# Optimization experiments

Hardware: AMD Instinct MI355X
Metric: run time of the kernel (lower is better)

The kernel has to match this reference:

```python
import jax, jax.numpy as jnp
import numpy as np

GRID_SIZE = 128
FEATURE_SIZE = 16
HIDDEN_SIZE = 64
N_POINTS = 2097152


def setup_inputs() -> dict:
    key = jax.random.key(0)
    ks = jax.random.split(key, 8)
    points = jax.random.uniform(ks[0], (N_POINTS, 3), dtype=jnp.float32)
    grid = jax.random.normal(ks[1], (GRID_SIZE, GRID_SIZE, GRID_SIZE, FEATURE_SIZE), dtype=jnp.float32)
    # torch nn.Linear default init: U(-1/sqrt(fan_in), 1/sqrt(fan_in))
    def linear(k, fan_in, fan_out):
        kw, kb = jax.random.split(k)
        bound = 1.0 / np.sqrt(fan_in)
        W = jax.random.uniform(kw, (fan_out, fan_in), minval=-bound, maxval=bound, dtype=jnp.float32)
        b = jax.random.uniform(kb, (fan_out,), minval=-bound, maxval=bound, dtype=jnp.float32)
        return W, b
    W1, b1 = linear(ks[2], FEATURE_SIZE, HIDDEN_SIZE)
    W2, b2 = linear(ks[3], HIDDEN_SIZE, HIDDEN_SIZE)
    W3, b3 = linear(ks[4], HIDDEN_SIZE, 1)
    return {"points": points, "grid": grid, "W1": W1, "b1": b1,
            "W2": W2, "b2": b2, "W3": W3, "b3": b3}


def reference(points, grid, W1, b1, W2, b2, W3, b3):
    gs = grid.shape[0]
    # nearest-grid-node index: scale to [0, gs-1], clamp, round
    p = jnp.clip(points * (gs - 1), 0.0, gs - 1)
    idx = jnp.round(p).astype(jnp.int32)  # (N, 3)
    feats = grid[idx[:, 0], idx[:, 1], idx[:, 2]]  # (N, F) gather
    h = jax.nn.relu(feats @ W1.T + b1)
    h = jax.nn.relu(h @ W2.T + b2)
    occ = jnp.tanh(h @ W3.T + b3)  # (N, 1)
    return occ
```

## Files before the change

kernel.cpp:

```cpp
#include <hip/hip_runtime.h>
#include <hip/hip_fp16.h>
#include <cstdint>
#include <cstddef>


typedef _Float16 half8 __attribute__((ext_vector_type(8)));
typedef float float4v __attribute__((ext_vector_type(4)));

__device__ inline uint32_t pack_f16x2(float a, float b) {
    union { _Float16 h[2]; uint32_t u; } v;
    v.h[0] = (_Float16)a;
    v.h[1] = (_Float16)b;
    return v.u;
}

__global__ __launch_bounds__(256) void occ_mlp_kernel(
    const float* __restrict__ pts,
    const float* __restrict__ grid,
    const float* __restrict__ W1, const float* __restrict__ b1,
    const float* __restrict__ W2, const float* __restrict__ b2,
    const float* __restrict__ W3, const float* __restrict__ b3,
    float* __restrict__ out, int nPoints)
{
    const int lane = threadIdx.x & 63;
    const int l15  = lane & 15;
    const int quad = lane >> 4;
    const int wavesPerBlock = blockDim.x >> 6;
    const int waveId = blockIdx.x * wavesPerBlock + (threadIdx.x >> 6);
    const int nWaves = gridDim.x * wavesPerBlock;

    half8 A1[4];
#pragma unroll
    for (int t = 0; t < 4; ++t) {
        half8 f = {};
        if (quad < 2) {
            const float* row = W1 + (16 * t + l15) * 16 + quad * 8;
#pragma unroll
            for (int j = 0; j < 8; ++j) f[j] = (_Float16)row[j];
        }
        A1[t] = f;
    }
    half8 A2[4][2];
#pragma unroll
    for (int t = 0; t < 4; ++t)
#pragma unroll
        for (int kk = 0; kk < 2; ++kk) {
            const float* row = W2 + (16 * t + l15) * 64 + 32 * kk + 8 * quad;
            half8 f;
#pragma unroll
            for (int j = 0; j < 8; ++j) f[j] = (_Float16)row[j];
            A2[t][kk] = f;
        }
    float4v bias1[4], bias2[4];
    float w3v[4][4];
#pragma unroll
    for (int t = 0; t < 4; ++t)
#pragma unroll
        for (int r = 0; r < 4; ++r) {
            int h = 16 * t + 4 * quad + r;
            bias1[t][r] = b1[h];
            bias2[t][r] = b2[h];
            w3v[t][r]   = W3[h];
        }
    const float bias3 = b3[0];

    const int src0 = l15 + 16 * ((2 * quad) & 3);
    const int src1 = l15 + 16 * ((2 * quad + 1) & 3);
    const bool sel = (quad >> 1) != 0;

    const int nTiles = (nPoints + 15) >> 4;
    for (int tile = waveId; tile < nTiles; tile += nWaves) {
        const int p = tile * 16 + l15;
        const int pc = p < nPoints ? p : nPoints - 1;

        const float px = pts[3 * pc + 0];
        const float py = pts[3 * pc + 1];
        const float pz = pts[3 * pc + 2];
        const int ix = (int)rintf(fminf(fmaxf(px * 127.0f, 0.0f), 127.0f));
        const int iy = (int)rintf(fminf(fmaxf(py * 127.0f, 0.0f), 127.0f));
        const int iz = (int)rintf(fminf(fmaxf(pz * 127.0f, 0.0f), 127.0f));
        const int ofs = ((((ix << 7) | iy) << 7) | iz) << 4;
        const float* g = grid + ofs;

        half8 bfrag = {};
        if (quad < 2) {
            const float4* gp = reinterpret_cast<const float4*>(g + quad * 8);
            const float4 f0 = gp[0];
            const float4 f1 = gp[1];
            bfrag[0] = (_Float16)f0.x; bfrag[1] = (_Float16)f0.y;
            bfrag[2] = (_Float16)f0.z; bfrag[3] = (_Float16)f0.w;
            bfrag[4] = (_Float16)f1.x; bfrag[5] = (_Float16)f1.y;
            bfrag[6] = (_Float16)f1.z; bfrag[7] = (_Float16)f1.w;
        }

        float4v C1[4];
#pragma unroll
        for (int t = 0; t < 4; ++t) {
            C1[t] = bias1[t];
            C1[t] = __builtin_amdgcn_mfma_f32_16x16x32_f16(A1[t], bfrag, C1[t], 0, 0, 0);
        }

        uint32_t P[4][2];
#pragma unroll
        for (int t = 0; t < 4; ++t) {
            const float v0 = fmaxf(C1[t][0], 0.0f);
            const float v1 = fmaxf(C1[t][1], 0.0f);
            const float v2 = fmaxf(C1[t][2], 0.0f);
            const float v3 = fmaxf(C1[t][3], 0.0f);
            P[t][0] = pack_f16x2(v0, v1);
            P[t][1] = pack_f16x2(v2, v3);
        }

        union Frag { uint32_t u[4]; half8 h; } B2[2];
#pragma unroll
        for (int kk = 0; kk < 2; ++kk) {
            const uint32_t x0a = (uint32_t)__shfl((int)P[2 * kk    ][0], src0);
            const uint32_t x0b = (uint32_t)__shfl((int)P[2 * kk + 1][0], src0);
            const uint32_t x1a = (uint32_t)__shfl((int)P[2 * kk    ][1], src0);
            const uint32_t x1b = (uint32_t)__shfl((int)P[2 * kk + 1][1], src0);
            const uint32_t y0a = (uint32_t)__shfl((int)P[2 * kk    ][0], src1);
            const uint32_t y0b = (uint32_t)__shfl((int)P[2 * kk + 1][0], src1);
            const uint32_t y1a = (uint32_t)__shfl((int)P[2 * kk    ][1], src1);
            const uint32_t y1b = (uint32_t)__shfl((int)P[2 * kk + 1][1], src1);
            B2[kk].u[0] = sel ? x0b : x0a;
            B2[kk].u[1] = sel ? x1b : x1a;
            B2[kk].u[2] = sel ? y0b : y0a;
            B2[kk].u[3] = sel ? y1b : y1a;
        }

        float4v C2[4];
#pragma unroll
        for (int t = 0; t < 4; ++t) C2[t] = bias2[t];
#pragma unroll
        for (int kk = 0; kk < 2; ++kk)
#pragma unroll
            for (int t = 0; t < 4; ++t)
                C2[t] = __builtin_amdgcn_mfma_f32_16x16x32_f16(A2[t][kk], B2[kk].h, C2[t], 0, 0, 0);

        float z = 0.0f;
#pragma unroll
        for (int t = 0; t < 4; ++t)
#pragma unroll
            for (int r = 0; r < 4; ++r)
                z = fmaf(fmaxf(C2[t][r], 0.0f), w3v[t][r], z);
        z += __shfl_xor(z, 16);
        z += __shfl_xor(z, 32);
        const float o = tanhf(z + bias3);
        if (lane < 16 && p < nPoints) out[p] = o;
    }
}

extern "C" void kernel_launch(void* const* d_in, const int* in_sizes, int n_in,
                              void* d_out, int out_size, void* d_ws, size_t ws_size,
                              hipStream_t stream)
{
    const float* pts  = (const float*)d_in[0];
    const float* grid = (const float*)d_in[1];
    const float* W1   = (const float*)d_in[2];
    const float* b1   = (const float*)d_in[3];
    const float* W2   = (const float*)d_in[4];
    const float* b2   = (const float*)d_in[5];
    const float* W3   = (const float*)d_in[6];
    const float* b3   = (const float*)d_in[7];
    float* out = (float*)d_out;
    const int nPoints = in_sizes[0] / 3;

    occ_mlp_kernel<<<dim3(2048), dim3(256), 0, stream>>>(
        pts, grid, W1, b1, W2, b2, W3, b3, out, nPoints);
}
```

Baseline: 286.7 us.

## Batch four point tiles per wave to overlap gathers and coalesce stores

Each wave now handles four 16-point tiles per iteration. It computes all four grid offsets and issues all eight random float4 gathers before any MFMA work, so more loads are in flight to hide gather latency. Outputs are collected so that all 64 lanes write one contiguous 64-float store, replacing four 16-lane stores. This raises register pressure from holding four tiles of gathered data, which may lower occupancy.

```diff
diff --git a/kernel.cpp b/kernel.cpp
--- a/kernel.cpp
+++ b/kernel.cpp
@@ -69,84 +69,102 @@
     const bool sel = (quad >> 1) != 0;
 
     const int nTiles = (nPoints + 15) >> 4;
-    for (int tile = waveId; tile < nTiles; tile += nWaves) {
-        const int p = tile * 16 + l15;
-        const int pc = p < nPoints ? p : nPoints - 1;
+    for (int tb = waveId * 4; tb < nTiles; tb += nWaves * 4) {
 
-        const float px = pts[3 * pc + 0];
-        const float py = pts[3 * pc + 1];
-        const float pz = pts[3 * pc + 2];
-        const int ix = (int)rintf(fminf(fmaxf(px * 127.0f, 0.0f), 127.0f));
-        const int iy = (int)rintf(fminf(fmaxf(py * 127.0f, 0.0f), 127.0f));
-        const int iz = (int)rintf(fminf(fmaxf(pz * 127.0f, 0.0f), 127.0f));
-        const int ofs = ((((ix << 7) | iy) << 7) | iz) << 4;
-        const float* g = grid + ofs;
-
-        half8 bfrag = {};
-        if (quad < 2) {
-            const float4* gp = reinterpret_cast<const float4*>(g + quad * 8);
-            const float4 f0 = gp[0];
-            const float4 f1 = gp[1];
-            bfrag[0] = (_Float16)f0.x; bfrag[1] = (_Float16)f0.y;
-            bfrag[2] = (_Float16)f0.z; bfrag[3] = (_Float16)f0.w;
-            bfrag[4] = (_Float16)f1.x; bfrag[5] = (_Float16)f1.y;
-            bfrag[6] = (_Float16)f1.z; bfrag[7] = (_Float16)f1.w;
+        int ofs[4];
+#pragma unroll
+        for (int u = 0; u < 4; ++u) {
+            int p = (tb + u) * 16 + l15;
+            int pc = p < nPoints ? p : nPoints - 1;
+            const float px = pts[3 * pc + 0];
+            const float py = pts[3 * pc + 1];
+            const float pz = pts[3 * pc + 2];
+            const int ix = (int)rintf(fminf(fmaxf(px * 127.0f, 0.0f), 127.0f));
+            const int iy = (int)rintf(fminf(fmaxf(py * 127.0f, 0.0f), 127.0f));
+            const int iz = (int)rintf(fminf(fmaxf(pz * 127.0f, 0.0f), 127.0f));
+            ofs[u] = ((((ix << 7) | iy) << 7) | iz) << 4;
         }
 
-        float4v C1[4];
+        float4 g0[4] = {}, g1[4] = {};
 #pragma unroll
-        for (int t = 0; t < 4; ++t) {
-            C1[t] = bias1[t];
-            C1[t] = __builtin_amdgcn_mfma_f32_16x16x32_f16(A1[t], bfrag, C1[t], 0, 0, 0);
+        for (int u = 0; u < 4; ++u) {
+            if (quad < 2) {
+                const float4* gp = reinterpret_cast<const float4*>(grid + ofs[u] + quad * 8);
+                g0[u] = gp[0];
+                g1[u] = gp[1];
+            }
         }
 
-        uint32_t P[4][2];
+        float o[4];
 #pragma unroll
-        for (int t = 0; t < 4; ++t) {
-            const float v0 = fmaxf(C1[t][0], 0.0f);
-            const float v1 = fmaxf(C1[t][1], 0.0f);
-            const float v2 = fmaxf(C1[t][2], 0.0f);
-            const float v3 = fmaxf(C1[t][3], 0.0f);
-            P[t][0] = pack_f16x2(v0, v1);
-            P[t][1] = pack_f16x2(v2, v3);
+        for (int u = 0; u < 4; ++u) {
+            half8 bfrag = {};
+            if (quad < 2) {
+                bfrag[0] = (_Float16)g0[u].x; bfrag[1] = (_Float16)g0[u].y;
+                bfrag[2] = (_Float16)g0[u].z; bfrag[3] = (_Float16)g0[u].w;
+                bfrag[4] = (_Float16)g1[u].x; bfrag[5] = (_Float16)g1[u].y;
+                bfrag[6] = (_Float16)g1[u].z; bfrag[7] = (_Float16)g1[u].w;
+            }
+
+            float4v C1[4];
+#pragma unroll
+            for (int t = 0; t < 4; ++t) {
+                C1[t] = bias1[t];
+                C1[t] = __builtin_amdgcn_mfma_f32_16x16x32_f16(A1[t], bfrag, C1[t], 0, 0, 0);
+            }
+
+            uint32_t P[4][2];
+#pragma unroll
+            for (int t = 0; t < 4; ++t) {
+                const float v0 = fmaxf(C1[t][0], 0.0f);
+                const float v1 = fmaxf(C1[t][1], 0.0f);
+                const float v2 = fmaxf(C1[t][2], 0.0f);
+                const float v3 = fmaxf(C1[t][3], 0.0f);
+                P[t][0] = pack_f16x2(v0, v1);
+                P[t][1] = pack_f16x2(v2, v3);
+            }
+
+            union Frag { uint32_t u[4]; half8 h; } B2[2];
+#pragma unroll
+            for (int kk = 0; kk < 2; ++kk) {
+                const uint32_t x0a = (uint32_t)__shfl((int)P[2 * kk    ][0], src0);
+                const uint32_t x0b = (uint32_t)__shfl((int)P[2 * kk + 1][0], src0);
+                const uint32_t x1a = (uint32_t)__shfl((int)P[2 * kk    ][1], src0);
+                const uint32_t x1b = (uint32_t)__shfl((int)P[2 * kk + 1][1], src0);
+                const uint32_t y0a = (uint32_t)__shfl((int)P[2 * kk    ][0], src1);
+                const uint32_t y0b = (uint32_t)__shfl((int)P[2 * kk + 1][0], src1);
+                const uint32_t y1a = (uint32_t)__shfl((int)P[2 * kk    ][1], src1);
+                const uint32_t y1b = (uint32_t)__shfl((int)P[2 * kk + 1][1], src1);
+                B2[kk].u[0] = sel ? x0b : x0a;
+                B2[kk].u[1] = sel ? x1b : x1a;
+                B2[kk].u[2] = sel ? y0b : y0a;
+                B2[kk].u[3] = sel ? y1b : y1a;
+            }
+
+            float4v C2[4];
+#pragma unroll
+            for (int t = 0; t < 4; ++t) C2[t] = bias2[t];
+#pragma unroll
+            for (int kk = 0; kk < 2; ++kk)
+#pragma unroll
+                for (int t = 0; t < 4; ++t)
+                    C2[t] = __builtin_amdgcn_mfma_f32_16x16x32_f16(A2[t][kk], B2[kk].h, C2[t], 0, 0, 0);
+
+            float z = 0.0f;
+#pragma unroll
+            for (int t = 0; t < 4; ++t)
+#pragma unroll
+                for (int r = 0; r < 4; ++r)
+                    z = fmaf(fmaxf(C2[t][r], 0.0f), w3v[t][r], z);
+            z += __shfl_xor(z, 16);
+            z += __shfl_xor(z, 32);
+            o[u] = tanhf(z + bias3);
         }
 
-        union Frag { uint32_t u[4]; half8 h; } B2[2];
-#pragma unroll
-        for (int kk = 0; kk < 2; ++kk) {
-            const uint32_t x0a = (uint32_t)__shfl((int)P[2 * kk    ][0], src0);
-            const uint32_t x0b = (uint32_t)__shfl((int)P[2 * kk + 1][0], src0);
-            const uint32_t x1a = (uint32_t)__shfl((int)P[2 * kk    ][1], src0);
-            const uint32_t x1b = (uint32_t)__shfl((int)P[2 * kk + 1][1], src0);
-            const uint32_t y0a = (uint32_t)__shfl((int)P[2 * kk    ][0], src1);
-            const uint32_t y0b = (uint32_t)__shfl((int)P[2 * kk + 1][0], src1);
-            const uint32_t y1a = (uint32_t)__shfl((int)P[2 * kk    ][1], src1);
-            const uint32_t y1b = (uint32_t)__shfl((int)P[2 * kk + 1][1], src1);
-            B2[kk].u[0] = sel ? x0b : x0a;
-            B2[kk].u[1] = sel ? x1b : x1a;
-            B2[kk].u[2] = sel ? y0b : y0a;
-            B2[kk].u[3] = sel ? y1b : y1a;
-        }
-
-        float4v C2[4];
-#pragma unroll
-        for (int t = 0; t < 4; ++t) C2[t] = bias2[t];
-#pragma unroll
-        for (int kk = 0; kk < 2; ++kk)
-#pragma unroll
-            for (int t = 0; t < 4; ++t)
-                C2[t] = __builtin_amdgcn_mfma_f32_16x16x32_f16(A2[t][kk], B2[kk].h, C2[t], 0, 0, 0);
-
-        float z = 0.0f;
-#pragma unroll
-        for (int t = 0; t < 4; ++t)
-#pragma unroll
-            for (int r = 0; r < 4; ++r)
-                z = fmaf(fmaxf(C2[t][r], 0.0f), w3v[t][r], z);
-        z += __shfl_xor(z, 16);
-        z += __shfl_xor(z, 32);
-        const float o = tanhf(z + bias3);
-        if (lane < 16 && p < nPoints) out[p] = o;
+        const float osel = (quad == 0) ? o[0] : (quad == 1) ? o[1]
+                         : (quad == 2) ? o[2] : o[3];
+        const int pstore = tb * 16 + lane;
+        if (pstore < nPoints) out[pstore] = osel;
     }
 }
 
```

New measurement: 271.6 us. 5.3% less time.

## Double-buffer grid gathers into LDS via async global_load_lds with chunked tiles

Applied to the files above, without the earlier changes.

Reworks the per-wave loop so each wave handles a fixed run of 16 tiles in chunks of 4. Grid feature rows are gathered asynchronously into double-buffered LDS with global_load_lds while the previous chunk runs through the MLP, and point coordinates are prefetched two chunks ahead. The layer-1 bias is folded into the MFMA through an extra ones column, tanh is replaced by an exp/rcp form, and outputs are written with one coalesced store per chunk. The launch also changes from a fixed grid-stride to an exact block count with occupancy hint 3, which adds LDS use and relies on the vmcnt(0) wait being correct.

```diff
diff --git a/kernel.cpp b/kernel.cpp
--- a/kernel.cpp
+++ b/kernel.cpp
@@ -6,6 +6,12 @@
 
 typedef _Float16 half8 __attribute__((ext_vector_type(8)));
 typedef float float4v __attribute__((ext_vector_type(4)));
+typedef __attribute__((address_space(3))) uint32_t lds_u32;
+typedef __attribute__((address_space(1))) const uint32_t glb_u32;
+
+#define WPB 4
+#define G   4
+#define NC  4
 
 __device__ inline uint32_t pack_f16x2(float a, float b) {
     union { _Float16 h[2]; uint32_t u; } v;
@@ -14,7 +20,7 @@
     return v.u;
 }
 
-__global__ __launch_bounds__(256) void occ_mlp_kernel(
+__global__ __launch_bounds__(256, 3) void occ_mlp_kernel(
     const float* __restrict__ pts,
     const float* __restrict__ grid,
     const float* __restrict__ W1, const float* __restrict__ b1,
@@ -22,12 +28,18 @@
     const float* __restrict__ W3, const float* __restrict__ b3,
     float* __restrict__ out, int nPoints)
 {
+    __shared__ float sbuf[WPB][2][G * 256];
+
     const int lane = threadIdx.x & 63;
     const int l15  = lane & 15;
     const int quad = lane >> 4;
-    const int wavesPerBlock = blockDim.x >> 6;
-    const int waveId = blockIdx.x * wavesPerBlock + (threadIdx.x >> 6);
-    const int nWaves = gridDim.x * wavesPerBlock;
+    const int wib  = threadIdx.x >> 6;
+    const int tile0 = (blockIdx.x * WPB + wib) * (G * NC);
+    const int nTiles = (nPoints + 15) >> 4;
+    if (tile0 >= nTiles) return;
+
+    float* const buf0 = &sbuf[wib][0][0];
+    float* const buf1 = &sbuf[wib][1][0];
 
     half8 A1[4];
 #pragma unroll
@@ -37,6 +49,8 @@
             const float* row = W1 + (16 * t + l15) * 16 + quad * 8;
 #pragma unroll
             for (int j = 0; j < 8; ++j) f[j] = (_Float16)row[j];
+        } else if (quad == 2) {
+            f[0] = (_Float16)b1[16 * t + l15];
         }
         A1[t] = f;
     }
@@ -51,14 +65,13 @@
             for (int j = 0; j < 8; ++j) f[j] = (_Float16)row[j];
             A2[t][kk] = f;
         }
-    float4v bias1[4], bias2[4];
+    float4v bias2[4];
     float w3v[4][4];
 #pragma unroll
     for (int t = 0; t < 4; ++t)
 #pragma unroll
         for (int r = 0; r < 4; ++r) {
             int h = 16 * t + 4 * quad + r;
-            bias1[t][r] = b1[h];
             bias2[t][r] = b2[h];
             w3v[t][r]   = W3[h];
         }
@@ -68,85 +81,121 @@
     const int src1 = l15 + 16 * ((2 * quad + 1) & 3);
     const bool sel = (quad >> 1) != 0;
 
-    const int nTiles = (nPoints + 15) >> 4;
-    for (int tile = waveId; tile < nTiles; tile += nWaves) {
-        const int p = tile * 16 + l15;
-        const int pc = p < nPoints ? p : nPoints - 1;
-
-        const float px = pts[3 * pc + 0];
-        const float py = pts[3 * pc + 1];
-        const float pz = pts[3 * pc + 2];
-        const int ix = (int)rintf(fminf(fmaxf(px * 127.0f, 0.0f), 127.0f));
-        const int iy = (int)rintf(fminf(fmaxf(py * 127.0f, 0.0f), 127.0f));
-        const int iz = (int)rintf(fminf(fmaxf(pz * 127.0f, 0.0f), 127.0f));
-        const int ofs = ((((ix << 7) | iy) << 7) | iz) << 4;
-        const float* g = grid + ofs;
-
-        half8 bfrag = {};
-        if (quad < 2) {
-            const float4* gp = reinterpret_cast<const float4*>(g + quad * 8);
-            const float4 f0 = gp[0];
-            const float4 f1 = gp[1];
-            bfrag[0] = (_Float16)f0.x; bfrag[1] = (_Float16)f0.y;
-            bfrag[2] = (_Float16)f0.z; bfrag[3] = (_Float16)f0.w;
-            bfrag[4] = (_Float16)f1.x; bfrag[5] = (_Float16)f1.y;
-            bfrag[6] = (_Float16)f1.z; bfrag[7] = (_Float16)f1.w;
-        }
-
-        float4v C1[4];
-#pragma unroll
-        for (int t = 0; t < 4; ++t) {
-            C1[t] = bias1[t];
-            C1[t] = __builtin_amdgcn_mfma_f32_16x16x32_f16(A1[t], bfrag, C1[t], 0, 0, 0);
-        }
-
-        uint32_t P[4][2];
-#pragma unroll
-        for (int t = 0; t < 4; ++t) {
-            const float v0 = fmaxf(C1[t][0], 0.0f);
-            const float v1 = fmaxf(C1[t][1], 0.0f);
-            const float v2 = fmaxf(C1[t][2], 0.0f);
-            const float v3 = fmaxf(C1[t][3], 0.0f);
-            P[t][0] = pack_f16x2(v0, v1);
-            P[t][1] = pack_f16x2(v2, v3);
-        }
-
-        union Frag { uint32_t u[4]; half8 h; } B2[2];
-#pragma unroll
-        for (int kk = 0; kk < 2; ++kk) {
-            const uint32_t x0a = (uint32_t)__shfl((int)P[2 * kk    ][0], src0);
-            const uint32_t x0b = (uint32_t)__shfl((int)P[2 * kk + 1][0], src0);
-            const uint32_t x1a = (uint32_t)__shfl((int)P[2 * kk    ][1], src0);
-            const uint32_t x1b = (uint32_t)__shfl((int)P[2 * kk + 1][1], src0);
-            const uint32_t y0a = (uint32_t)__shfl((int)P[2 * kk    ][0], src1);
-            const uint32_t y0b = (uint32_t)__shfl((int)P[2 * kk + 1][0], src1);
-            const uint32_t y1a = (uint32_t)__shfl((int)P[2 * kk    ][1], src1);
-            const uint32_t y1b = (uint32_t)__shfl((int)P[2 * kk + 1][1], src1);
-            B2[kk].u[0] = sel ? x0b : x0a;
-            B2[kk].u[1] = sel ? x1b : x1a;
-            B2[kk].u[2] = sel ? y0b : y0a;
-            B2[kk].u[3] = sel ? y1b : y1a;
-        }
-
-        float4v C2[4];
-#pragma unroll
-        for (int t = 0; t < 4; ++t) C2[t] = bias2[t];
-#pragma unroll
-        for (int kk = 0; kk < 2; ++kk)
+    const int gpt  = lane >> 2;
+    const int gseg = lane & 3;
+    const int maxP = nPoints - 1;
+
+    float Rx[G], Ry[G], Rz[G];
+
+    auto loadChunkPts = [&](int c) {
+#pragma unroll
+        for (int u = 0; u < G; ++u) {
+            int p = (tile0 + c * G + u) * 16 + gpt;
+            p = p > maxP ? maxP : p;
+            const float* q = pts + 3 * p;
+            Rx[u] = q[0]; Ry[u] = q[1]; Rz[u] = q[2];
+        }
+    };
+    auto dmaChunk = [&](float* buf) {
+#pragma unroll
+        for (int u = 0; u < G; ++u) {
+            const int ix = (int)rintf(fminf(fmaxf(Rx[u] * 127.0f, 0.0f), 127.0f));
+            const int iy = (int)rintf(fminf(fmaxf(Ry[u] * 127.0f, 0.0f), 127.0f));
+            const int iz = (int)rintf(fminf(fmaxf(Rz[u] * 127.0f, 0.0f), 127.0f));
+            const int ofs = ((((ix << 7) | iy) << 7) | iz) << 4;
+            const float* ga = grid + ofs + (gseg << 2);
+            __builtin_amdgcn_global_load_lds((glb_u32*)ga,
+                                             (lds_u32*)(buf + u * 256), 16, 0, 0);
+        }
+    };
+
+    loadChunkPts(0);
+    dmaChunk(buf0);
+    loadChunkPts(1);
+
+#pragma unroll
+    for (int k = 0; k < NC; ++k) {
+        float* const bufC = (k & 1) ? buf1 : buf0;
+        float* const bufN = (k & 1) ? buf0 : buf1;
+
+        asm volatile("s_waitcnt vmcnt(0)" ::: "memory");
+
+        if (k + 1 < NC) dmaChunk(bufN);
+        if (k + 2 < NC) loadChunkPts(k + 2);
+
+        float o[G];
+#pragma unroll
+        for (int u = 0; u < G; ++u) {
+            half8 bfrag = {};
+            if (quad < 2) {
+                const float4* gp = reinterpret_cast<const float4*>(
+                    bufC + u * 256 + (l15 << 4) + (quad << 3));
+                const float4 f0 = gp[0];
+                const float4 f1 = gp[1];
+                bfrag[0] = (_Float16)f0.x; bfrag[1] = (_Float16)f0.y;
+                bfrag[2] = (_Float16)f0.z; bfrag[3] = (_Float16)f0.w;
+                bfrag[4] = (_Float16)f1.x; bfrag[5] = (_Float16)f1.y;
+                bfrag[6] = (_Float16)f1.z; bfrag[7] = (_Float16)f1.w;
+            } else if (quad == 2) {
+                bfrag[0] = (_Float16)1.0f;
+            }
+
+            float4v C1[4];
+#pragma unroll
+            for (int t = 0; t < 4; ++t) {
+                float4v zacc = {};
+                C1[t] = __builtin_amdgcn_mfma_f32_16x16x32_f16(A1[t], bfrag, zacc, 0, 0, 0);
+            }
+
+            uint32_t P[4][2];
+#pragma unroll
+            for (int t = 0; t < 4; ++t) {
+                P[t][0] = pack_f16x2(fmaxf(C1[t][0], 0.0f), fmaxf(C1[t][1], 0.0f));
+                P[t][1] = pack_f16x2(fmaxf(C1[t][2], 0.0f), fmaxf(C1[t][3], 0.0f));
+            }
+
+            union Frag { uint32_t u[4]; half8 h; } B2[2];
+#pragma unroll
+            for (int kk = 0; kk < 2; ++kk) {
+                const uint32_t x0a = (uint32_t)__shfl((int)P[2 * kk    ][0], src0);
+                const uint32_t x0b = (uint32_t)__shfl((int)P[2 * kk + 1][0], src0);
+                const uint32_t x1a = (uint32_t)__shfl((int)P[2 * kk    ][1], src0);
+                const uint32_t x1b = (uint32_t)__shfl((int)P[2 * kk + 1][1], src0);
+                const uint32_t y0a = (uint32_t)__shfl((int)P[2 * kk    ][0], src1);
+                const uint32_t y0b = (uint32_t)__shfl((int)P[2 * kk + 1][0], src1);
+                const uint32_t y1a = (uint32_t)__shfl((int)P[2 * kk    ][1], src1);
+                const uint32_t y1b = (uint32_t)__shfl((int)P[2 * kk + 1][1], src1);
+                B2[kk].u[0] = sel ? x0b : x0a;
+                B2[kk].u[1] = sel ? x1b : x1a;
+                B2[kk].u[2] = sel ? y0b : y0a;
+                B2[kk].u[3] = sel ? y1b : y1a;
+            }
+
+            float4v C2[4];
+#pragma unroll
+            for (int t = 0; t < 4; ++t) C2[t] = bias2[t];
+#pragma unroll
+            for (int kk = 0; kk < 2; ++kk)
+#pragma unroll
+                for (int t = 0; t < 4; ++t)
+                    C2[t] = __builtin_amdgcn_mfma_f32_16x16x32_f16(A2[t][kk], B2[kk].h, C2[t], 0, 0, 0);
+
+            float z = 0.0f;
 #pragma unroll
             for (int t = 0; t < 4; ++t)
-                C2[t] = __builtin_amdgcn_mfma_f32_16x16x32_f16(A2[t][kk], B2[kk].h, C2[t], 0, 0, 0);
-
-        float z = 0.0f;
-#pragma unroll
-        for (int t = 0; t < 4; ++t)
-#pragma unroll
-            for (int r = 0; r < 4; ++r)
-                z = fmaf(fmaxf(C2[t][r], 0.0f), w3v[t][r], z);
-        z += __shfl_xor(z, 16);
-        z += __shfl_xor(z, 32);
-        const float o = tanhf(z + bias3);
-        if (lane < 16 && p < nPoints) out[p] = o;
+#pragma unroll
+                for (int r = 0; r < 4; ++r)
+                    z = fmaf(fmaxf(C2[t][r], 0.0f), w3v[t][r], z);
+            z += __shfl_xor(z, 16);
+            z += __shfl_xor(z, 32);
+            const float e = __expf(2.0f * (z + bias3));
+            o[u] = fmaf(-2.0f, __builtin_amdgcn_rcpf(e + 1.0f), 1.0f);
+        }
+
+        const float osel = (quad == 0) ? o[0] : (quad == 1) ? o[1]
+                         : (quad == 2) ? o[2] : o[3];
+        const int pstore = (tile0 + k * G) * 16 + lane;
+        if (pstore <= maxP) out[pstore] = osel;
     }
 }
 
@@ -165,6 +214,10 @@
     float* out = (float*)d_out;
     const int nPoints = in_sizes[0] / 3;
 
-    occ_mlp_kernel<<<dim3(2048), dim3(256), 0, stream>>>(
+    const int nTiles = (nPoints + 15) >> 4;
+    const int tilesPerBlock = WPB * G * NC;
+    const int nBlocks = (nTiles + tilesPerBlock - 1) / tilesPerBlock;
+
+    occ_mlp_kernel<<<dim3(nBlocks), dim3(256), 0, stream>>>(
         pts, grid, W1, b1, W2, b2, W3, b3, out, nPoints);
 }
```

Result: faster. 258.3 us (-9.9%).
